# Optimization experiments

Measured on AMD Instinct MI355X. Metric: run time of the kernel, lower is better.

The kernel has to match this reference:

```python
import jax, jax.numpy as jnp
import numpy as np

NUM_HEADS = 16


def setup_inputs() -> dict:
    key = jax.random.key(0)
    ks = jax.random.split(key, 8)
    B, N, C = 2, 1024, 1024
    H, D = NUM_HEADS, C // NUM_HEADS
    Npast = 8192
    s = 0.02
    return {
        "x": jax.random.normal(ks[0], (B, N, C), jnp.float32),
        "past_k": jax.random.normal(ks[1], (B, H, Npast, D), jnp.float32),
        "past_v": jax.random.normal(ks[2], (B, H, Npast, D), jnp.float32),
        "qkv_w": jax.random.normal(ks[3], (3 * C, C), jnp.float32) * s,
        "qkv_b": jax.random.normal(ks[4], (3 * C,), jnp.float32) * s,
        "proj_w": jax.random.normal(ks[5], (C, C), jnp.float32) * s,
        "proj_b": jax.random.normal(ks[6], (C,), jnp.float32) * s,
        "cache_budget": 4096,
    }


def reference(x, past_k, past_v, qkv_w, qkv_b, proj_w, proj_b, cache_budget):
    B, N, C = x.shape
    H = NUM_HEADS
    D = C // H
    scale = D ** -0.5

    # fused QKV projection -> [3, B, H, N, D]
    qkv = (x @ qkv_w.T + qkv_b).reshape(B, N, 3, H, D).transpose(2, 0, 3, 1, 4)
    q, k, v = qkv[0], qkv[1], qkv[2]

    # use_cache path: anchor tokens = current-frame token count on first call
    num_anchor = N
    k = jnp.concatenate([past_k, k], axis=2)  # [B,H,Ntot,D]
    v = jnp.concatenate([past_v, v], axis=2)
    Ntot = k.shape[2]

    # eviction: mean cosine-similarity scoring over candidate (non-anchor) keys.
    # mean_j cos(k_i, k_j) == khat_i . mean_j(khat_j) -- O(N*D), no NxN matrix.
    num_keep = cache_budget - num_anchor
    cand_k = k[:, :, num_anchor:, :]  # [B,H,Ncand,D]
    khat = cand_k / (jnp.linalg.norm(cand_k, axis=-1, keepdims=True) + 1e-6)
    mean_dir = khat.mean(axis=2, keepdims=True)
    mean_scores = (khat * mean_dir).sum(-1)  # [B,H,Ncand]
    # keep the least-redundant tokens (lowest mean similarity)
    _, top_idx = jax.lax.top_k(-mean_scores, num_keep)  # [B,H,num_keep]
    top_idx = jnp.sort(top_idx, axis=-1)
    avg_scores = mean_scores.mean()

    anchor_idx = jnp.broadcast_to(jnp.arange(num_anchor)[None, None, :], (B, H, num_anchor))
    keep_idx = jnp.concatenate([anchor_idx, top_idx + num_anchor], axis=2)  # [B,H,budget]
    gidx = keep_idx[..., None]
    k_new = jnp.take_along_axis(k, jnp.broadcast_to(gidx, (B, H, cache_budget, D)), axis=2)
    v_new = jnp.take_along_axis(v, jnp.broadcast_to(gidx, (B, H, cache_budget, D)), axis=2)

    # SDPA
    logits = jnp.einsum("bhqd,bhkd->bhqk", q, k_new) * scale
    attn = jax.nn.softmax(logits, axis=-1)
    o = jnp.einsum("bhqk,bhkd->bhqd", attn, v_new)
    o = o.transpose(0, 2, 1, 3).reshape(B, N, C)
    out = o @ proj_w.T + proj_b
    return out, k_new, v_new, avg_scores
```

## Files before the change

### kernel.cpp

```cpp
#include <hip/hip_runtime.h>
#include <hip/hip_bf16.h>
#include <math.h>

#define BB 2
#define HH 16
#define NN 1024
#define CC 1024
#define DD 64
#define NPAST 8192
#define NANCH 1024
#define CBUD 4096
#define NKEEP 3072
#define NCAND 8192
#define BH 32

#define TILEB 16384

#define OUT_SZ   (BB*NN*CC)
#define KNEW_OFF ((size_t)OUT_SZ)
#define KNEW_SZ  ((size_t)BH*CBUD*DD)
#define VNEW_OFF (KNEW_OFF + KNEW_SZ)
#define AVG_OFF  (VNEW_OFF + KNEW_SZ)

#define WS_KF   ((size_t)0)
#define WS_VF   ((size_t)2097152)
#define WS_VT   ((size_t)0)
#define WS_XT   ((size_t)4194304)
#define WS_OT   ((size_t)4194304)
#define WS_WQVT ((size_t)5242880)
#define WS_WPT  ((size_t)5242880)
#define WS_QB   ((size_t)6291456)
#define WS_MD   ((size_t)7340032)
#define WS_SC   ((size_t)7342080)
#define WS_BS   ((size_t)7604224)
#define WS_SEL  ((size_t)7604288)
#define WS_MDP  ((size_t)7702592)
#define WS_BSP  ((size_t)7718976)

typedef __attribute__((ext_vector_type(8))) short short8;
typedef __attribute__((ext_vector_type(4))) float f32x4;

typedef unsigned int __attribute__((address_space(3))) lds_uint;
typedef unsigned int __attribute__((address_space(1))) glb_uint;

__device__ __forceinline__ void gload16(const void* g, void* l) {
    __builtin_amdgcn_global_load_lds((const glb_uint*)g, (lds_uint*)l, 16, 0, 0);
}

__device__ inline unsigned short f2bf(float f) {
    unsigned u = __float_as_uint(f);
    unsigned r = (u + 0x7FFFu + ((u >> 16) & 1u)) >> 16;
    return (unsigned short)r;
}
__device__ inline unsigned cvtpk(float a, float b) {
    __hip_bfloat162 h = __float22bfloat162_rn(make_float2(a, b));
    return *reinterpret_cast<unsigned*>(&h);
}
__device__ __forceinline__ float fexp2(float x) {
#if __has_builtin(__builtin_amdgcn_exp2f)
    return __builtin_amdgcn_exp2f(x);
#else
    return exp2f(x);
#endif
}

__global__ __launch_bounds__(256) void conv_tile(const float* __restrict__ src,
                                                 unsigned short* __restrict__ dst)
{
    int gid = blockIdx.x * 256 + threadIdx.x;
    int r = gid >> 7, k0 = (gid & 127) * 8;
    float4 a = *(const float4*)&src[(size_t)r * 1024 + k0];
    float4 b = *(const float4*)&src[(size_t)r * 1024 + k0 + 4];
    uint4 u;
    u.x = cvtpk(a.x, a.y); u.y = cvtpk(a.z, a.w);
    u.z = cvtpk(b.x, b.y); u.w = cvtpk(b.z, b.w);
    size_t tile = (size_t)(r >> 7) * 16 + (k0 >> 6);
    int inner = (((r & 127) * 128 + (k0 & 63) * 2)) ^ ((r & 7) << 4);
    *(uint4*)((char*)dst + tile * TILEB + inner) = u;
}

__global__ __launch_bounds__(256) void conv_wqv(const float* __restrict__ src,
                                                unsigned short* __restrict__ dst)
{
    int gid = blockIdx.x * 256 + threadIdx.x;
    int n = gid >> 7, k0 = (gid & 127) * 8;
    int srow = (n < 1024) ? n : n + 1024;
    float4 a = *(const float4*)&src[(size_t)srow * 1024 + k0];
    float4 b = *(const float4*)&src[(size_t)srow * 1024 + k0 + 4];
    uint4 u;
    u.x = cvtpk(a.x, a.y); u.y = cvtpk(a.z, a.w);
    u.z = cvtpk(b.x, b.y); u.w = cvtpk(b.z, b.w);
    size_t tile = (size_t)(n >> 7) * 16 + (k0 >> 6);
    int inner = (((n & 127) * 128 + (k0 & 63) * 2)) ^ ((n & 7) << 4);
    *(uint4*)((char*)dst + tile * TILEB + inner) = u;
}

__global__ __launch_bounds__(256) void kf_gemm(const float* __restrict__ x,
                                               const float* __restrict__ w,
                                               const float* __restrict__ bias,
                                               float* __restrict__ ws)
{
    __shared__ float As[16][68];
    __shared__ float Bs[16][68];
    int tid = threadIdx.x;
    int m0 = blockIdx.y * 64;
    int n0 = blockIdx.x * 64;
    int tx = tid & 15, ty = tid >> 4;
    int lr = tid >> 2;
    int lk = (tid & 3) * 4;
    float acc[4][4] = {{0.f}};

    float4 a = *(const float4*)&x[(size_t)(m0 + lr) * CC + lk];
    float4 b = *(const float4*)&w[(size_t)(1024 + n0 + lr) * CC + lk];

    for (int k0 = 0; k0 < CC; k0 += 16) {
        __syncthreads();
        As[lk+0][lr] = a.x; As[lk+1][lr] = a.y; As[lk+2][lr] = a.z; As[lk+3][lr] = a.w;
        Bs[lk+0][lr] = b.x; Bs[lk+1][lr] = b.y; Bs[lk+2][lr] = b.z; Bs[lk+3][lr] = b.w;
        __syncthreads();
        if (k0 + 16 < CC) {
            a = *(const float4*)&x[(size_t)(m0 + lr) * CC + k0 + 16 + lk];
            b = *(const float4*)&w[(size_t)(1024 + n0 + lr) * CC + k0 + 16 + lk];
        }
        float tacc[4][4] = {{0.f}};
        #pragma unroll
        for (int kk = 0; kk < 16; ++kk) {
            float4 a4 = *(const float4*)&As[kk][ty*4];
            float4 b4 = *(const float4*)&Bs[kk][tx*4];
            float av[4] = {a4.x, a4.y, a4.z, a4.w};
            float bv[4] = {b4.x, b4.y, b4.z, b4.w};
            #pragma unroll
            for (int i = 0; i < 4; ++i)
                #pragma unroll
                for (int j = 0; j < 4; ++j)
                    tacc[i][j] += av[i] * bv[j];
        }
        #pragma unroll
        for (int i = 0; i < 4; ++i)
            #pragma unroll
            for (int j = 0; j < 4; ++j)
                acc[i][j] += tacc[i][j];
    }

    int cn0 = n0 + tx * 4;
    int h = cn0 >> 6, dd0 = cn0 & 63;
    float4 b4 = *(const float4*)&bias[1024 + cn0];
    float* kf = ws + WS_KF;
    #pragma unroll
    for (int i = 0; i < 4; ++i) {
        int m = m0 + ty * 4 + i;
        int b2 = m >> 10, n = m & 1023;
        float4 t;
        t.x = acc[i][0] + b4.x; t.y = acc[i][1] + b4.y;
        t.z = acc[i][2] + b4.z; t.w = acc[i][3] + b4.w;
        *(float4*)&kf[(((size_t)b2*HH + h)*NN + n)*DD + dd0] = t;
    }
}

template<int MODE>
__global__ __launch_bounds__(256) void mfma_gemm(const unsigned short* __restrict__ At,
                                                 const unsigned short* __restrict__ Bt,
                                                 const float* __restrict__ bias,
                                                 float* __restrict__ outp)
{
    __shared__ char lds[131072];
    int tid = threadIdx.x;
    int w = tid >> 6, lane = tid & 63;
    int g = lane >> 4, r16 = lane & 15;
    int wr = w >> 1, wc = w & 1;
    int bm = blockIdx.y, bn = blockIdx.x;
    const int KB = 16;

    f32x4 acc[4][4];
    #pragma unroll
    for (int i = 0; i < 4; ++i)
        #pragma unroll
        for (int j = 0; j < 4; ++j) acc[i][j] = 0.f;

    const char* Abase = (const char*)At + (size_t)bm * KB * TILEB;
    const char* Bbase = (const char*)Bt + (size_t)bn * KB * TILEB;

    #pragma unroll
    for (int i = 0; i < 4; ++i) {
        gload16(Abase + (size_t)w*4096 + i*1024 + lane*16, lds + w*4096 + i*1024);
        gload16(Bbase + (size_t)w*4096 + i*1024 + lane*16, lds + TILEB + w*4096 + i*1024);
    }
    asm volatile("s_waitcnt vmcnt(0)" ::: "memory");
    __syncthreads();

    int cur = 0;
    for (int kb = 0; kb < KB; ++kb) {
        char* Acur = lds + cur * (2*TILEB);
        char* Bcur = Acur + TILEB;
        if (kb + 1 < KB) {
            char* Anxt = lds + (cur ^ 1) * (2*TILEB);
            char* Bnxt = Anxt + TILEB;
            const char* an = Abase + (size_t)(kb+1)*TILEB + w*4096;
            const char* bsrc = Bbase + (size_t)(kb+1)*TILEB + w*4096;
            #pragma unroll
            for (int i = 0; i < 4; ++i) {
                gload16(an + i*1024 + lane*16, Anxt + w*4096 + i*1024);
                gload16(bsrc + i*1024 + lane*16, Bnxt + w*4096 + i*1024);
            }
        }
        short8 a0[4], a1[4], b0[4], b1[4];
        #pragma unroll
        for (int mi = 0; mi < 4; ++mi) {
            int row = wr*64 + mi*16 + r16;
            int sw = (row & 7) << 4;
            a0[mi] = *(const short8*)(Acur + ((row*128 + g*16) ^ sw));
            a1[mi] = *(const short8*)(Acur + ((row*128 + 64 + g*16) ^ sw));
        }
        #pragma unroll
        for (int ni = 0; ni < 4; ++ni) {
            int row = wc*64 + ni*16 + r16;
            int sw = (row & 7) << 4;
            b0[ni] = *(const short8*)(Bcur + ((row*128 + g*16) ^ sw));
            b1[ni] = *(const short8*)(Bcur + ((row*128 + 64 + g*16) ^ sw));
        }
        __builtin_amdgcn_s_setprio(1);
        #pragma unroll
        for (int mi = 0; mi < 4; ++mi)
            #pragma unroll
            for (int ni = 0; ni < 4; ++ni) {
                acc[mi][ni] = __builtin_amdgcn_mfma_f32_16x16x32_bf16(a0[mi], b0[ni], acc[mi][ni], 0, 0, 0);
                acc[mi][ni] = __builtin_amdgcn_mfma_f32_16x16x32_bf16(a1[mi], b1[ni], acc[mi][ni], 0, 0, 0);
            }
        __builtin_amdgcn_s_setprio(0);
        asm volatile("s_waitcnt vmcnt(0)" ::: "memory");
        __syncthreads();
        cur ^= 1;
    }

    int nq = bn*128 + wc*64;
    float bv[4];
    #pragma unroll
    for (int ni = 0; ni < 4; ++ni) {
        int n = nq + ni*16 + r16;
        bv[ni] = (MODE == 0) ? bias[(n < 1024) ? n : (n + 1024)] : bias[n];
    }
    #pragma unroll
    for (int mi = 0; mi < 4; ++mi) {
        #pragma unroll
        for (int rr = 0; rr < 4; ++rr) {
            int ml = wr*64 + mi*16 + 4*g + rr;
            int mg = bm*128 + ml;
            int bb = mg >> 10, tok = mg & 1023;
            #pragma unroll
            for (int ni = 0; ni < 4; ++ni) {
                int n = nq + ni*16 + r16;
                float v = acc[mi][ni][rr] + bv[ni];
                if (MODE == 0) {
                    if (n < 1024) {
                        unsigned short* qb = (unsigned short*)(outp + WS_QB);
                        int hh = n >> 6, d = n & 63;
                        qb[(((size_t)bb*16 + hh)*1024 + tok)*64 + d] = f2bf(v);
                    } else {
                        float* vf = outp + WS_VF;
                        int hh = (n - 1024) >> 6, d = n & 63;
                        vf[(((size_t)bb*16 + hh)*1024 + tok)*64 + d] = v;
                    }
                } else {
                    outp[(size_t)mg*1024 + n] = v;
                }
            }
        }
    }
}

__global__ __launch_bounds__(256) void meandir_part(const float* __restrict__ past_k,
                                                    float* __restrict__ ws)
{
    int bh = blockIdx.x, seg = blockIdx.y, tid = threadIdx.x;
    const float* kpast = past_k + (size_t)bh * NPAST * DD;
    const float* knew  = ws + WS_KF + (size_t)bh * NN * DD;
    float dir[64];
    #pragma unroll
    for (int i = 0; i < 64; ++i) dir[i] = 0.f;

    int j0 = seg * 1024;
    for (int jj = tid; jj < 1024; jj += 256) {
        int pos = NANCH + j0 + jj;
        const float* row = (pos < NPAST) ? (kpast + (size_t)pos * DD)
                                         : (knew + (size_t)(pos - NPAST) * DD);
        float v[64]; float ss = 0.f;
        #pragma unroll
        for (int g = 0; g < 16; ++g) {
            float4 t = *(const float4*)&row[g*4];
            v[4*g]=t.x; v[4*g+1]=t.y; v[4*g+2]=t.z; v[4*g+3]=t.w;
            ss += t.x*t.x + t.y*t.y + t.z*t.z + t.w*t.w;
        }
        float inv = 1.0f / (sqrtf(ss) + 1e-6f);
        #pragma unroll
        for (int i = 0; i < 64; ++i) dir[i] += v[i] * inv;
    }
    #pragma unroll
    for (int i = 0; i < 64; ++i)
        for (int off = 32; off; off >>= 1) dir[i] += __shfl_xor(dir[i], off);

    __shared__ float sdir[4][64];
    int lane = tid & 63, wid = tid >> 6;
    if (lane == 0) {
        #pragma unroll
        for (int i = 0; i < 64; ++i) sdir[wid][i] = dir[i];
    }
    __syncthreads();
    if (tid < 64) {
        float s = sdir[0][tid] + sdir[1][tid] + sdir[2][tid] + sdir[3][tid];
        ws[WS_MDP + ((size_t)bh*8 + seg)*DD + tid] = s;
    }
}

__global__ void meandir_red(float* __restrict__ ws)
{
    int bh = blockIdx.x, tid = threadIdx.x;
    float s = 0.f;
    #pragma unroll
    for (int seg = 0; seg < 8; ++seg)
        s += ws[WS_MDP + ((size_t)bh*8 + seg)*DD + tid];
    ws[WS_MD + (size_t)bh*DD + tid] = s * (1.0f / (float)NCAND);
}

__global__ __launch_bounds__(256) void scores_part(const float* __restrict__ past_k,
                                                   float* __restrict__ ws)
{
    __shared__ float md[64];
    __shared__ float sred[4];
    int bh = blockIdx.x, seg = blockIdx.y, tid = threadIdx.x;
    if (tid < 64) md[tid] = ws[WS_MD + (size_t)bh*DD + tid];
    __syncthreads();
    const float* kpast = past_k + (size_t)bh * NPAST * DD;
    const float* knew  = ws + WS_KF + (size_t)bh * NN * DD;
    float ssum = 0.f;
    int j0 = seg * 1024;
    for (int jj = tid; jj < 1024; jj += 256) {
        int j = j0 + jj;
        int pos = NANCH + j;
        const float* row = (pos < NPAST) ? (kpast + (size_t)pos * DD)
                                         : (knew + (size_t)(pos - NPAST) * DD);
        float ss = 0.f, dp = 0.f;
        #pragma unroll
        for (int g = 0; g < 16; ++g) {
            float4 t = *(const float4*)&row[g*4];
            ss += t.x*t.x + t.y*t.y + t.z*t.z + t.w*t.w;
            dp += t.x*md[4*g] + t.y*md[4*g+1] + t.z*md[4*g+2] + t.w*md[4*g+3];
        }
        float sc = dp / (sqrtf(ss) + 1e-6f);
        ws[WS_SC + (size_t)bh*NCAND + j] = sc;
        ssum += sc;
    }
    for (int off = 32; off; off >>= 1) ssum += __shfl_xor(ssum, off);
    int lane = tid & 63, wid = tid >> 6;
    if (lane == 0) sred[wid] = ssum;
    __syncthreads();
    if (tid == 0)
        ws[WS_BSP + (size_t)bh*8 + seg] = sred[0] + sred[1] + sred[2] + sred[3];
}

__global__ void avg_k(const float* __restrict__ ws, float* __restrict__ dout)
{
    __shared__ float red[4];
    int tid = threadIdx.x;
    float v = ws[WS_BSP + tid];
    for (int off = 32; off; off >>= 1) v += __shfl_xor(v, off);
    int lane = tid & 63, wid = tid >> 6;
    if (lane == 0) red[wid] = v;
    __syncthreads();
    if (tid == 0)
        dout[AVG_OFF] = (red[0]+red[1]+red[2]+red[3]) * (1.0f / ((float)BH * (float)NCAND));
}

__global__ __launch_bounds__(1024) void topk_k(float* __restrict__ ws, int* __restrict__ sel)
{
    __shared__ unsigned keys[NCAND];
    __shared__ int hist[256];
    __shared__ int red[16];
    __shared__ int red2[16];
    __shared__ int bcast;
    __shared__ unsigned bbyte;
    int bh = blockIdx.x, tid = threadIdx.x;
    int lane = tid & 63, wid = tid >> 6;

    for (int j = tid; j < NCAND; j += 1024) {
        unsigned u = __float_as_uint(ws[WS_SC + (size_t)bh*NCAND + j]);
        u ^= (u & 0x80000000u) ? 0xFFFFFFFFu : 0x80000000u;
        keys[j] = u;
    }
    __syncthreads();

    int rem = NKEEP;
    unsigned prefix = 0;
    #pragma unroll
    for (int pass = 0; pass < 4; ++pass) {
        int shift = 24 - 8*pass;
        if (tid < 256) hist[tid] = 0;
        __syncthreads();
        unsigned himask = (pass == 0) ? 0u : (0xFFFFFFFFu << (shift + 8));
        for (int j = tid; j < NCAND; j += 1024) {
            unsigned k = keys[j];
            if ((k & himask) == prefix)
                atomicAdd(&hist[(k >> shift) & 255], 1);
        }
        __syncthreads();
        if (tid == 0) {
            int cum = 0, b = 0;
            for (; b < 255; ++b) {
                if (rem <= cum + hist[b]) break;
                cum += hist[b];
            }
            bcast = cum;
            bbyte = (unsigned)b;
        }
        __syncthreads();
        rem -= bcast;
        prefix |= (bbyte << shift);
        __syncthreads();
    }
    unsigned T = prefix;

    {
        int cnt = 0;
        for (int j = tid; j < NCAND; j += 1024) cnt += (int)(keys[j] < T);
        for (int off = 32; off; off >>= 1) cnt += __shfl_xor(cnt, off);
        if (lane == 0) red[wid] = cnt;
        __syncthreads();
        if (tid == 0) { int c = 0; for (int i = 0; i < 16; ++i) c += red[i]; bcast = c; }
        __syncthreads();
    }
    int c_less = bcast;
    int ttie = NKEEP - c_less;

    int base = tid * 8;
    unsigned kv[8]; int lcnt = 0, ecnt = 0;
    #pragma unroll
    for (int i = 0; i < 8; ++i) {
        kv[i] = keys[base + i];
        lcnt += (int)(kv[i] < T);
        ecnt += (int)(kv[i] == T);
    }
    int li = lcnt, ei = ecnt;
    for (int off = 1; off < 64; off <<= 1) {
        int tl = __shfl_up(li, off);
        int te = __shfl_up(ei, off);
        if (lane >= off) { li += tl; ei += te; }
    }
    __syncthreads();
    if (lane == 63) { red[wid] = li; red2[wid] = ei; }
    __syncthreads();
    int lb = 0, eb = 0;
    for (int w = 0; w < wid; ++w) { lb += red[w]; eb += red2[w]; }
    lb += li - lcnt; eb += ei - ecnt;
    #pragma unroll
    for (int i = 0; i < 8; ++i) {
        bool less = kv[i] < T, eq = kv[i] == T;
        if (less || (eq && eb < ttie)) {
            int pos = lb + (eb < ttie ? eb : ttie);
            sel[(size_t)bh*NKEEP + pos] = base + i;
        }
        lb += (int)less; eb += (int)eq;
    }
}

__global__ __launch_bounds__(256) void gather_k(const float* __restrict__ past_k,
                                                const float* __restrict__ past_v,
                                                const float* __restrict__ ws,
                                                const int* __restrict__ sel,
                                                float* __restrict__ dout)
{
    int gid = blockIdx.x * 256 + threadIdx.x;
    int row = gid >> 4, lane = gid & 15;
    int bh = row >> 12, r = row & 4095;
    int pos = (r < NANCH) ? r : (NANCH + sel[(size_t)bh*NKEEP + (r - NANCH)]);
    const float *kr, *vr;
    if (pos < NPAST) {
        kr = past_k + ((size_t)bh*NPAST + pos) * DD;
        vr = past_v + ((size_t)bh*NPAST + pos) * DD;
    } else {
        kr = ws + WS_KF + ((size_t)bh*NN + (pos - NPAST)) * DD;
        vr = ws + WS_VF + ((size_t)bh*NN + (pos - NPAST)) * DD;
    }
    float4 kq = *(const float4*)&kr[lane*4];
    float4 vq = *(const float4*)&vr[lane*4];
    *(float4*)&dout[KNEW_OFF + ((size_t)bh*CBUD + r)*DD + lane*4] = kq;
    *(float4*)&dout[VNEW_OFF + ((size_t)bh*CBUD + r)*DD + lane*4] = vq;
}

__global__ __launch_bounds__(256) void vtrans_k(const float* __restrict__ dout,
                                                unsigned short* __restrict__ vt)
{
    __shared__ unsigned short S[64][65];
    int bh = blockIdx.x >> 6, kt = blockIdx.x & 63;
    int c0 = kt * 64;
    int tid = threadIdx.x;
    int r = tid >> 2, c4 = (tid & 3) * 16;
    const float* src = dout + VNEW_OFF + ((size_t)bh*CBUD + c0 + r)*DD + c4;
    #pragma unroll
    for (int i = 0; i < 4; ++i) {
        float4 f = *(const float4*)&src[i*4];
        S[r][c4 + i*4 + 0] = f2bf(f.x);
        S[r][c4 + i*4 + 1] = f2bf(f.y);
        S[r][c4 + i*4 + 2] = f2bf(f.z);
        S[r][c4 + i*4 + 3] = f2bf(f.w);
    }
    __syncthreads();
    int d = r, k4 = c4;
    uint4 u0, u1;
    u0.x = (unsigned)S[k4+0][d] | ((unsigned)S[k4+1][d] << 16);
    u0.y = (unsigned)S[k4+2][d] | ((unsigned)S[k4+3][d] << 16);
    u0.z = (unsigned)S[k4+4][d] | ((unsigned)S[k4+5][d] << 16);
    u0.w = (unsigned)S[k4+6][d] | ((unsigned)S[k4+7][d] << 16);
    u1.x = (unsigned)S[k4+8][d] | ((unsigned)S[k4+9][d] << 16);
    u1.y = (unsigned)S[k4+10][d] | ((unsigned)S[k4+11][d] << 16);
    u1.z = (unsigned)S[k4+12][d] | ((unsigned)S[k4+13][d] << 16);
    u1.w = (unsigned)S[k4+14][d] | ((unsigned)S[k4+15][d] << 16);
    unsigned short* dst = vt + ((size_t)bh*DD + d)*CBUD + c0 + k4;
    *(uint4*)&dst[0] = u0;
    *(uint4*)&dst[8] = u1;
}

__global__ __launch_bounds__(256) void attn_mfma(const unsigned short* __restrict__ qb,
                                                 const float* __restrict__ dout,
                                                 const unsigned short* __restrict__ vt,
                                                 unsigned short* __restrict__ ot)
{
    __shared__ char kls[2][8192];
    __shared__ char vls[2][8192];
    __shared__ char pls[4][2048];

    const float SCL = 0.125f * 1.44269504089f;
    const float THR = 11.5415603f;

    int orig = blockIdx.x;
    int bid = (orig & 7) * 64 + (orig >> 3);
    int bh = bid >> 4, qt = bid & 15;
    int b = bh >> 4, h = bh & 15;
    int tid = threadIdx.x;
    int w = tid >> 6, lane = tid & 63;
    int g = lane >> 4, r16 = lane & 15;
    int q0 = qt * 64 + w * 16;

    const unsigned short* qrow = qb + ((size_t)bh*NN + q0 + r16) * DD;
    short8 qa0 = *(const short8*)&qrow[8*g];
    short8 qa1 = *(const short8*)&qrow[32 + 8*g];

    const float* kf = dout + KNEW_OFF + (size_t)bh * CBUD * DD;
    const unsigned short* vtb = vt + (size_t)bh * DD * CBUD;
    char* plw = pls[w];
    int psw = (r16 & 7) << 4;

    int srA = tid >> 3;
    int srB = srA + 32;
    int scb = (tid & 7) * 16;
    int d0  = scb >> 1;
    int sdA = (srA*128 + scb) ^ ((srA & 7) << 4);
    int sdB = (srB*128 + scb) ^ ((srB & 7) << 4);

    f32x4 accd[4];
    #pragma unroll
    for (int dt = 0; dt < 4; ++dt) accd[dt] = 0.f;
    float m = -3.0e38f, l = 0.f;

    {
        const float* ksA = kf + (size_t)srA * DD + d0;
        const float* ksB = kf + (size_t)srB * DD + d0;
        float4 a0 = *(const float4*)ksA, a1 = *(const float4*)(ksA + 4);
        float4 b0 = *(const float4*)ksB, b1 = *(const float4*)(ksB + 4);
        uint4 kuA, kuB;
        kuA.x = cvtpk(a0.x,a0.y); kuA.y = cvtpk(a0.z,a0.w);
        kuA.z = cvtpk(a1.x,a1.y); kuA.w = cvtpk(a1.z,a1.w);
        kuB.x = cvtpk(b0.x,b0.y); kuB.y = cvtpk(b0.z,b0.w);
        kuB.z = cvtpk(b1.x,b1.y); kuB.w = cvtpk(b1.z,b1.w);
        uint4 vuA = *(const uint4*)(vtb + (size_t)srA*CBUD + d0);
        uint4 vuB = *(const uint4*)(vtb + (size_t)srB*CBUD + d0);
        *(uint4*)&kls[0][sdA] = kuA; *(uint4*)&kls[0][sdB] = kuB;
        *(uint4*)&vls[0][sdA] = vuA; *(uint4*)&vls[0][sdB] = vuB;
    }
    __syncthreads();

    int cur = 0;
    for (int t = 0; t < 64; ++t) {
        float4 a0, a1, b0, b1; uint4 vuA, vuB;
        bool more = (t + 1 < 64);
        if (more) {
            const float* ksA = kf + (size_t)(t+1)*64*DD + (size_t)srA * DD + d0;
            const float* ksB = kf + (size_t)(t+1)*64*DD + (size_t)srB * DD + d0;
            a0 = *(const float4*)ksA; a1 = *(const float4*)(ksA + 4);
            b0 = *(const float4*)ksB; b1 = *(const float4*)(ksB + 4);
            vuA = *(const uint4*)(vtb + (size_t)srA*CBUD + (t+1)*64 + d0);
            vuB = *(const uint4*)(vtb + (size_t)srB*CBUD + (t+1)*64 + d0);
        }

        const char* kb = kls[cur];
        f32x4 sacc[4];
        #pragma unroll
        for (int t4 = 0; t4 < 4; ++t4) sacc[t4] = 0.f;
        __builtin_amdgcn_s_setprio(1);
        #pragma unroll
        for (int t4 = 0; t4 < 4; ++t4) {
            int row = 16*t4 + r16;
            int sw = (r16 & 7) << 4;
            short8 ka0 = *(const short8*)(kb + ((row*128 + g*16) ^ sw));
            short8 ka1 = *(const short8*)(kb + ((row*128 + 64 + g*16) ^ sw));
            sacc[t4] = __builtin_amdgcn_mfma_f32_16x16x32_bf16(ka0, qa0, sacc[t4], 0, 0, 0);
            sacc[t4] = __builtin_amdgcn_mfma_f32_16x16x32_bf16(ka1, qa1, sacc[t4], 0, 0, 0);
        }
        __builtin_amdgcn_s_setprio(0);

        float sv[4][4];
        float smax = -3.0e38f;
        #pragma unroll
        for (int t4 = 0; t4 < 4; ++t4)
            #pragma unroll
            for (int rr = 0; rr < 4; ++rr) {
                sv[t4][rr] = sacc[t4][rr] * SCL;
                smax = fmaxf(smax, sv[t4][rr]);
            }
        smax = fmaxf(smax, __shfl_xor(smax, 16));
        smax = fmaxf(smax, __shfl_xor(smax, 32));

        if (!__all(smax <= m + THR)) {
            float mnew = fmaxf(m, smax);
            float rs = fexp2(m - mnew);
            l *= rs;
            m = mnew;
            float rq0 = __shfl(rs, 20*g + 0);
            float rq1 = __shfl(rs, 20*g + 1);
            float rq2 = __shfl(rs, 20*g + 2);
            float rq3 = __shfl(rs, 20*g + 3);
            #pragma unroll
            for (int dt = 0; dt < 4; ++dt) {
                accd[dt][0] *= rq0; accd[dt][1] *= rq1;
                accd[dt][2] *= rq2; accd[dt][3] *= rq3;
            }
        }

        float ps = 0.f;
        float p[4][4];
        #pragma unroll
        for (int t4 = 0; t4 < 4; ++t4)
            #pragma unroll
            for (int rr = 0; rr < 4; ++rr) {
                p[t4][rr] = fexp2(sv[t4][rr] - m);
                ps += p[t4][rr];
            }
        #pragma unroll
        for (int t4 = 0; t4 < 4; ++t4) {
            unsigned u0 = cvtpk(p[t4][0], p[t4][1]);
            unsigned u1 = cvtpk(p[t4][2], p[t4][3]);
            int cb = (16*t4 + 4*g) * 2;
            *(unsigned*)&plw[(r16*128 + cb)     ^ psw] = u0;
            *(unsigned*)&plw[(r16*128 + cb + 4) ^ psw] = u1;
        }
        ps += __shfl_xor(ps, 16);
        ps += __shfl_xor(ps, 32);
        l += ps;

        short8 pa0 = *(const short8*)&plw[(r16*128 + 16*g)      ^ psw];
        short8 pa1 = *(const short8*)&plw[(r16*128 + 64 + 16*g) ^ psw];
        const char* vb = vls[cur];
        __builtin_amdgcn_s_setprio(1);
        #pragma unroll
        for (int dt = 0; dt < 4; ++dt) {
            int row = dt*16 + r16;
            int sw = (r16 & 7) << 4;
            short8 vb0 = *(const short8*)(vb + ((row*128 + g*16) ^ sw));
            short8 vb1 = *(const short8*)(vb + ((row*128 + 64 + g*16) ^ sw));
            accd[dt] = __builtin_amdgcn_mfma_f32_16x16x32_bf16(pa0, vb0, accd[dt], 0, 0, 0);
            accd[dt] = __builtin_amdgcn_mfma_f32_16x16x32_bf16(pa1, vb1, accd[dt], 0, 0, 0);
        }
        __builtin_amdgcn_s_setprio(0);

        if (more) {
            uint4 kuA, kuB;
            kuA.x = cvtpk(a0.x,a0.y); kuA.y = cvtpk(a0.z,a0.w);
            kuA.z = cvtpk(a1.x,a1.y); kuA.w = cvtpk(a1.z,a1.w);
            kuB.x = cvtpk(b0.x,b0.y); kuB.y = cvtpk(b0.z,b0.w);
            kuB.z = cvtpk(b1.x,b1.y); kuB.w = cvtpk(b1.z,b1.w);
            *(uint4*)&kls[cur^1][sdA] = kuA; *(uint4*)&kls[cur^1][sdB] = kuB;
            *(uint4*)&vls[cur^1][sdA] = vuA; *(uint4*)&vls[cur^1][sdB] = vuB;
        }
        __syncthreads();
        cur ^= 1;
    }

    float ivl = 1.0f / l;
    float iq0 = __shfl(ivl, 20*g + 0);
    float iq1 = __shfl(ivl, 20*g + 1);
    float iq2 = __shfl(ivl, 20*g + 2);
    float iq3 = __shfl(ivl, 20*g + 3);
    float iq[4] = {iq0, iq1, iq2, iq3};
    #pragma unroll
    for (int dt = 0; dt < 4; ++dt) {
        #pragma unroll
        for (int rr = 0; rr < 4; ++rr) {
            int q = q0 + 4*g + rr;
            int mrow = b*1024 + q;
            int d = dt*16 + r16;
            size_t tile = (size_t)(mrow >> 7) * 16 + h;
            int inner = ((mrow & 127)*128 + d*2) ^ ((mrow & 7) << 4);
            *(unsigned short*)((char*)ot + tile*TILEB + inner) = f2bf(accd[dt][rr] * iq[rr]);
        }
    }
}

extern "C" void kernel_launch(void* const* d_in, const int* in_sizes, int n_in,
                              void* d_out, int out_size, void* d_ws, size_t ws_size,
                              hipStream_t stream)
{
    (void)in_sizes; (void)n_in; (void)out_size; (void)ws_size;
    const float* x      = (const float*)d_in[0];
    const float* past_k = (const float*)d_in[1];
    const float* past_v = (const float*)d_in[2];
    const float* qkv_w  = (const float*)d_in[3];
    const float* qkv_b  = (const float*)d_in[4];
    const float* proj_w = (const float*)d_in[5];
    const float* proj_b = (const float*)d_in[6];
    float* out = (float*)d_out;
    float* ws  = (float*)d_ws;
    int*   sel = (int*)(ws + WS_SEL);
    unsigned short* xt   = (unsigned short*)(ws + WS_XT);
    unsigned short* wqvt = (unsigned short*)(ws + WS_WQVT);
    unsigned short* wpt  = (unsigned short*)(ws + WS_WPT);
    unsigned short* qbp  = (unsigned short*)(ws + WS_QB);
    unsigned short* vtp  = (unsigned short*)(ws + WS_VT);
    unsigned short* otp  = (unsigned short*)(ws + WS_OT);

    conv_tile<<<1024, 256, 0, stream>>>(x, xt);
    conv_wqv<<<1024, 256, 0, stream>>>(qkv_w, wqvt);
    kf_gemm<<<dim3(16, 32), 256, 0, stream>>>(x, qkv_w, qkv_b, ws);
    mfma_gemm<0><<<dim3(16, 16), 256, 0, stream>>>(xt, wqvt, qkv_b, ws);
    meandir_part<<<dim3(32, 8), 256, 0, stream>>>(past_k, ws);
    meandir_red<<<32, 64, 0, stream>>>(ws);
    scores_part<<<dim3(32, 8), 256, 0, stream>>>(past_k, ws);
    avg_k<<<1, 256, 0, stream>>>(ws, out);
    topk_k<<<32, 1024, 0, stream>>>(ws, sel);
    gather_k<<<8192, 256, 0, stream>>>(past_k, past_v, ws, sel, out);
    vtrans_k<<<2048, 256, 0, stream>>>(out, vtp);
    conv_tile<<<512, 256, 0, stream>>>(proj_w, wpt);
    attn_mfma<<<512, 256, 0, stream>>>(qbp, out, vtp, otp);
    mfma_gemm<1><<<dim3(8, 16), 256, 0, stream>>>(otp, wpt, proj_b, out);
}
```

Before: 303.4 us.

## Split attention over KV halves with combine kernel and pre-swizzled V tiles

Splits each attention block's 4096-key loop into two halves processed by separate blocks, so the grid doubles to 1024 blocks for better CU occupancy. Partial unnormalized outputs go to scratch in bf16 (reusing the output buffer region) with per-row max/sum, and a new combine kernel merges them. V is now stored by the transpose kernel as pre-swizzled 8KB tiles so attention can load it with direct global-to-LDS loads instead of register staging. This adds a combine pass, extra memory traffic and bf16 rounding of partials, and it writes scratch into the output buffer before the final GEMM overwrites it.

```diff
diff --git a/kernel.cpp b/kernel.cpp
--- a/kernel.cpp
+++ b/kernel.cpp
@@ -24,7 +24,7 @@
 
 #define WS_KF   ((size_t)0)
 #define WS_VF   ((size_t)2097152)
-#define WS_VT   ((size_t)0)
+#define WS_VTS  ((size_t)0)
 #define WS_XT   ((size_t)4194304)
 #define WS_OT   ((size_t)4194304)
 #define WS_WQVT ((size_t)5242880)
@@ -32,6 +32,7 @@
 #define WS_QB   ((size_t)6291456)
 #define WS_MD   ((size_t)7340032)
 #define WS_SC   ((size_t)7342080)
+#define WS_ML   WS_SC
 #define WS_BS   ((size_t)7604224)
 #define WS_SEL  ((size_t)7604288)
 #define WS_MDP  ((size_t)7702592)
@@ -62,6 +63,9 @@
 #else
     return exp2f(x);
 #endif
+}
+__device__ __forceinline__ float bf2f(unsigned short u) {
+    return __uint_as_float((unsigned)u << 16);
 }
 
 __global__ __launch_bounds__(256) void conv_tile(const float* __restrict__ src,
@@ -513,15 +517,16 @@
     u1.y = (unsigned)S[k4+10][d] | ((unsigned)S[k4+11][d] << 16);
     u1.z = (unsigned)S[k4+12][d] | ((unsigned)S[k4+13][d] << 16);
     u1.w = (unsigned)S[k4+14][d] | ((unsigned)S[k4+15][d] << 16);
-    unsigned short* dst = vt + ((size_t)bh*DD + d)*CBUD + c0 + k4;
-    *(uint4*)&dst[0] = u0;
-    *(uint4*)&dst[8] = u1;
-}
-
-__global__ __launch_bounds__(256) void attn_mfma(const unsigned short* __restrict__ qb,
-                                                 const float* __restrict__ dout,
-                                                 const unsigned short* __restrict__ vt,
-                                                 unsigned short* __restrict__ ot)
+    size_t tbase = ((size_t)bh*64 + kt) * 8192;
+    int sw = (d & 7) << 4;
+    *(uint4*)((char*)vt + tbase + ((d*128 + k4*2)      ^ sw)) = u0;
+    *(uint4*)((char*)vt + tbase + ((d*128 + k4*2 + 16) ^ sw)) = u1;
+}
+
+__global__ __launch_bounds__(256) void attn_split(const unsigned short* __restrict__ qb,
+                                                  float* __restrict__ dout,
+                                                  const unsigned short* __restrict__ vt,
+                                                  float* __restrict__ ws)
 {
     __shared__ char kls[2][8192];
     __shared__ char vls[2][8192];
@@ -531,20 +536,22 @@
     const float THR = 11.5415603f;
 
     int orig = blockIdx.x;
-    int bid = (orig & 7) * 64 + (orig >> 3);
-    int bh = bid >> 4, qt = bid & 15;
-    int b = bh >> 4, h = bh & 15;
+    int bid = (orig & 7) * 128 + (orig >> 3);
+    int bh = bid >> 5;
+    int qt = (bid >> 1) & 15;
+    int half = bid & 1;
     int tid = threadIdx.x;
     int w = tid >> 6, lane = tid & 63;
     int g = lane >> 4, r16 = lane & 15;
     int q0 = qt * 64 + w * 16;
+    int t0 = half * 32;
 
     const unsigned short* qrow = qb + ((size_t)bh*NN + q0 + r16) * DD;
     short8 qa0 = *(const short8*)&qrow[8*g];
     short8 qa1 = *(const short8*)&qrow[32 + 8*g];
 
     const float* kf = dout + KNEW_OFF + (size_t)bh * CBUD * DD;
-    const unsigned short* vtb = vt + (size_t)bh * DD * CBUD;
+    const char* vtt = (const char*)vt + (size_t)bh * 64 * 8192;
     char* plw = pls[w];
     int psw = (r16 & 7) << 4;
 
@@ -561,8 +568,10 @@
     float m = -3.0e38f, l = 0.f;
 
     {
-        const float* ksA = kf + (size_t)srA * DD + d0;
-        const float* ksB = kf + (size_t)srB * DD + d0;
+        gload16(vtt + (size_t)t0*8192 + tid*16,        vls[0] + tid*16);
+        gload16(vtt + (size_t)t0*8192 + 4096 + tid*16, vls[0] + 4096 + tid*16);
+        const float* ksA = kf + ((size_t)t0*64 + srA) * DD + d0;
+        const float* ksB = kf + ((size_t)t0*64 + srB) * DD + d0;
         float4 a0 = *(const float4*)ksA, a1 = *(const float4*)(ksA + 4);
         float4 b0 = *(const float4*)ksB, b1 = *(const float4*)(ksB + 4);
         uint4 kuA, kuB;
@@ -570,24 +579,21 @@
         kuA.z = cvtpk(a1.x,a1.y); kuA.w = cvtpk(a1.z,a1.w);
         kuB.x = cvtpk(b0.x,b0.y); kuB.y = cvtpk(b0.z,b0.w);
         kuB.z = cvtpk(b1.x,b1.y); kuB.w = cvtpk(b1.z,b1.w);
-        uint4 vuA = *(const uint4*)(vtb + (size_t)srA*CBUD + d0);
-        uint4 vuB = *(const uint4*)(vtb + (size_t)srB*CBUD + d0);
         *(uint4*)&kls[0][sdA] = kuA; *(uint4*)&kls[0][sdB] = kuB;
-        *(uint4*)&vls[0][sdA] = vuA; *(uint4*)&vls[0][sdB] = vuB;
     }
     __syncthreads();
 
     int cur = 0;
-    for (int t = 0; t < 64; ++t) {
-        float4 a0, a1, b0, b1; uint4 vuA, vuB;
-        bool more = (t + 1 < 64);
+    for (int t = t0; t < t0 + 32; ++t) {
+        float4 a0, a1, b0, b1;
+        bool more = (t + 1 < t0 + 32);
         if (more) {
-            const float* ksA = kf + (size_t)(t+1)*64*DD + (size_t)srA * DD + d0;
-            const float* ksB = kf + (size_t)(t+1)*64*DD + (size_t)srB * DD + d0;
+            gload16(vtt + (size_t)(t+1)*8192 + tid*16,        vls[cur^1] + tid*16);
+            gload16(vtt + (size_t)(t+1)*8192 + 4096 + tid*16, vls[cur^1] + 4096 + tid*16);
+            const float* ksA = kf + ((size_t)(t+1)*64 + srA) * DD + d0;
+            const float* ksB = kf + ((size_t)(t+1)*64 + srB) * DD + d0;
             a0 = *(const float4*)ksA; a1 = *(const float4*)(ksA + 4);
             b0 = *(const float4*)ksB; b1 = *(const float4*)(ksB + 4);
-            vuA = *(const uint4*)(vtb + (size_t)srA*CBUD + (t+1)*64 + d0);
-            vuB = *(const uint4*)(vtb + (size_t)srB*CBUD + (t+1)*64 + d0);
         }
 
         const char* kb = kls[cur];
@@ -645,11 +651,11 @@
             }
         #pragma unroll
         for (int t4 = 0; t4 < 4; ++t4) {
-            unsigned u0 = cvtpk(p[t4][0], p[t4][1]);
-            unsigned u1 = cvtpk(p[t4][2], p[t4][3]);
+            uint2 u;
+            u.x = cvtpk(p[t4][0], p[t4][1]);
+            u.y = cvtpk(p[t4][2], p[t4][3]);
             int cb = (16*t4 + 4*g) * 2;
-            *(unsigned*)&plw[(r16*128 + cb)     ^ psw] = u0;
-            *(unsigned*)&plw[(r16*128 + cb + 4) ^ psw] = u1;
+            *(uint2*)&plw[(r16*128 + cb) ^ psw] = u;
         }
         ps += __shfl_xor(ps, 16);
         ps += __shfl_xor(ps, 32);
@@ -677,30 +683,65 @@
             kuB.x = cvtpk(b0.x,b0.y); kuB.y = cvtpk(b0.z,b0.w);
             kuB.z = cvtpk(b1.x,b1.y); kuB.w = cvtpk(b1.z,b1.w);
             *(uint4*)&kls[cur^1][sdA] = kuA; *(uint4*)&kls[cur^1][sdB] = kuB;
-            *(uint4*)&vls[cur^1][sdA] = vuA; *(uint4*)&vls[cur^1][sdB] = vuB;
         }
         __syncthreads();
         cur ^= 1;
     }
 
-    float ivl = 1.0f / l;
-    float iq0 = __shfl(ivl, 20*g + 0);
-    float iq1 = __shfl(ivl, 20*g + 1);
-    float iq2 = __shfl(ivl, 20*g + 2);
-    float iq3 = __shfl(ivl, 20*g + 3);
-    float iq[4] = {iq0, iq1, iq2, iq3};
-    #pragma unroll
-    for (int dt = 0; dt < 4; ++dt) {
-        #pragma unroll
-        for (int rr = 0; rr < 4; ++rr) {
-            int q = q0 + 4*g + rr;
-            int mrow = b*1024 + q;
-            int d = dt*16 + r16;
-            size_t tile = (size_t)(mrow >> 7) * 16 + h;
-            int inner = ((mrow & 127)*128 + d*2) ^ ((mrow & 7) << 4);
-            *(unsigned short*)((char*)ot + tile*TILEB + inner) = f2bf(accd[dt][rr] * iq[rr]);
-        }
-    }
+    unsigned short* po = (unsigned short*)dout;
+    size_t pq = ((size_t)half*BH + bh)*NN;
+    #pragma unroll
+    for (int dt = 0; dt < 4; ++dt)
+        #pragma unroll
+        for (int rr = 0; rr < 4; ++rr)
+            po[(pq + q0 + 4*g + rr)*DD + dt*16 + r16] = f2bf(accd[dt][rr]);
+    if (g == 0) {
+        float2* mlp = (float2*)(ws + WS_ML);
+        mlp[pq + q0 + r16] = make_float2(m, l);
+    }
+}
+
+__global__ __launch_bounds__(256) void combine_k(const float* __restrict__ dout,
+                                                 const float* __restrict__ ws,
+                                                 unsigned short* __restrict__ ot)
+{
+    int gid = blockIdx.x * 256 + threadIdx.x;
+    int d8 = gid & 7;
+    int q  = (gid >> 3) & 1023;
+    int bh = gid >> 13;
+
+    const float2* mlp = (const float2*)(ws + WS_ML);
+    float2 ml0 = mlp[((size_t)0*BH + bh)*NN + q];
+    float2 ml1 = mlp[((size_t)1*BH + bh)*NN + q];
+    float mm = fmaxf(ml0.x, ml1.x);
+    float w0 = fexp2(ml0.x - mm), w1 = fexp2(ml1.x - mm);
+    float inv = 1.0f / (w0*ml0.y + w1*ml1.y);
+    float s0 = w0 * inv, s1 = w1 * inv;
+
+    const unsigned short* po = (const unsigned short*)dout;
+    const unsigned short* a0 = po + (((size_t)0*BH + bh)*NN + q)*DD + d8*8;
+    const unsigned short* a1 = po + (((size_t)1*BH + bh)*NN + q)*DD + d8*8;
+    uint4 u0 = *(const uint4*)a0;
+    uint4 u1 = *(const uint4*)a1;
+
+    unsigned r[4];
+    const unsigned* p0 = (const unsigned*)&u0;
+    const unsigned* p1 = (const unsigned*)&u1;
+    #pragma unroll
+    for (int i = 0; i < 4; ++i) {
+        float lo = bf2f((unsigned short)(p0[i] & 0xFFFF)) * s0
+                 + bf2f((unsigned short)(p1[i] & 0xFFFF)) * s1;
+        float hi = bf2f((unsigned short)(p0[i] >> 16)) * s0
+                 + bf2f((unsigned short)(p1[i] >> 16)) * s1;
+        r[i] = cvtpk(lo, hi);
+    }
+
+    int b = bh >> 4, h = bh & 15;
+    int mrow = b*1024 + q;
+    size_t tile = (size_t)(mrow >> 7) * 16 + h;
+    int inner = ((mrow & 127)*128 + d8*16) ^ ((mrow & 7) << 4);
+    uint4 out4; out4.x = r[0]; out4.y = r[1]; out4.z = r[2]; out4.w = r[3];
+    *(uint4*)((char*)ot + tile*TILEB + inner) = out4;
 }
 
 extern "C" void kernel_launch(void* const* d_in, const int* in_sizes, int n_in,
@@ -722,7 +763,7 @@
     unsigned short* wqvt = (unsigned short*)(ws + WS_WQVT);
     unsigned short* wpt  = (unsigned short*)(ws + WS_WPT);
     unsigned short* qbp  = (unsigned short*)(ws + WS_QB);
-    unsigned short* vtp  = (unsigned short*)(ws + WS_VT);
+    unsigned short* vtp  = (unsigned short*)(ws + WS_VTS);
     unsigned short* otp  = (unsigned short*)(ws + WS_OT);
 
     conv_tile<<<1024, 256, 0, stream>>>(x, xt);
@@ -737,6 +778,7 @@
     gather_k<<<8192, 256, 0, stream>>>(past_k, past_v, ws, sel, out);
     vtrans_k<<<2048, 256, 0, stream>>>(out, vtp);
     conv_tile<<<512, 256, 0, stream>>>(proj_w, wpt);
-    attn_mfma<<<512, 256, 0, stream>>>(qbp, out, vtp, otp);
+    attn_split<<<1024, 256, 0, stream>>>(qbp, out, vtp, ws);
+    combine_k<<<1024, 256, 0, stream>>>(out, ws, otp);
     mfma_gemm<1><<<dim3(8, 16), 256, 0, stream>>>(otp, wpt, proj_b, out);
 }
```

Result: slower. 321.7 us (+6.0%).
